# Kernel optimization log

Measured on AMD Instinct MI355X. Metric: run time of the kernel, lower is better.

Reference implementation:

```python
import jax, jax.numpy as jnp
import numpy as np

ALPHA = 1.702
LIMIT = 7.0

# Tiling: A*B*M = BD*S (total dispatched tokens)
A, B, E, M, H, I = 2, 8, 16, 128, 2048, 2048
_BD, _S = 2, 1024


def setup_inputs() -> dict:
    key = jax.random.key(0)
    ks = jax.random.split(key, 6)
    inv_h = 1.0 / np.sqrt(H)
    inv_i = 1.0 / np.sqrt(I)
    return {
        "dispatched": jax.random.normal(ks[0], (A, B, E, M, H), dtype=jnp.float32),
        "gate_up_proj": jax.random.normal(ks[1], (E, H, 2 * I), dtype=jnp.float32) * inv_h,
        "gate_up_proj_bias": jax.random.normal(ks[2], (E, 2 * I), dtype=jnp.float32) * 0.02,
        "down_proj": jax.random.normal(ks[3], (E, I, H), dtype=jnp.float32) * inv_i,
        "down_proj_bias": jax.random.normal(ks[4], (E, H), dtype=jnp.float32) * 0.02,
        "sparsity_remap": jax.random.randint(ks[5], (E, E), 0, E, dtype=jnp.int32),
        "BD": _BD,
        "S": _S,
    }


def _moe_activation_gpt_oss(gate_up_out):
    # interleaved gate/up: [g0,u0,g1,u1,...]
    gate = gate_up_out[..., ::2]
    up = gate_up_out[..., 1::2]
    gate = jnp.minimum(gate, LIMIT)
    up = jnp.clip(up, -LIMIT, LIMIT)
    glu = gate * jax.nn.sigmoid(gate * ALPHA)
    return (up + 1.0) * glu


def reference(dispatched, gate_up_proj, gate_up_proj_bias, down_proj,
              down_proj_bias, sparsity_remap, BD, S):
    # sparsity_remap is an opaque tile remap for tt.sparse_matmul; the dense
    # grouped matmul computes the same math (zero tiles contribute zeros).
    a, b, e, m, h = dispatched.shape
    inter = gate_up_proj.shape[-1] // 2
    # grouped gate_up GEMM: [A,B,E,M,H] @ [E,H,2I] -> [A,B,E,M,2I]
    gate_up_out = jnp.einsum('abemh,ehn->abemn', dispatched, gate_up_proj)
    gate_up_out = gate_up_out + gate_up_proj_bias[None, None, :, None, :]
    activated = _moe_activation_gpt_oss(gate_up_out)  # [A,B,E,M,I]
    activated = activated.reshape(a * b, e, m, inter)
    # grouped down GEMM: [AB,E,M,I] @ [E,I,H] -> [AB,E,M,H]
    down_out = jnp.einsum('xemi,eih->xemh', activated, down_proj)
    down_out = down_out + down_proj_bias[None, :, None, :]
    # untile: [AB,E,M,H] -> [AB,M,E,H] -> [BD,S,E,H]
    down_out = jnp.transpose(down_out, (0, 2, 1, 3))
    return down_out.reshape(BD, S, e, h)
```

## Files before the change

kernel.cpp:

```cpp
#include <hip/hip_runtime.h>
#include <stdint.h>

#define DEV __device__ __forceinline__

constexpr int E_ = 16, M_ = 128, H_ = 2048, I_ = 2048;
constexpr int X_ = 16;
constexpr int N1 = 2 * I_;
constexpr int ROWS = X_ * M_;

typedef short bfrag __attribute__((ext_vector_type(8)));
typedef float ffrag __attribute__((ext_vector_type(4)));
typedef unsigned short us8 __attribute__((ext_vector_type(8)));

DEV unsigned short f2bf(float f) {
    union { float f; unsigned u; } v; v.f = f;
    unsigned u = v.u;
    u += 0x7fffu + ((u >> 16) & 1u);
    return (unsigned short)(u >> 16);
}

DEV void gload16(const void* g, void* lds_wave_base) {
    __builtin_amdgcn_global_load_lds(
        (const __attribute__((address_space(1))) unsigned int*)g,
        (__attribute__((address_space(3))) unsigned int*)lds_wave_base,
        16, 0, 0);
}

DEV void block_bar() {
    asm volatile("" ::: "memory");
    __builtin_amdgcn_s_barrier();
    asm volatile("" ::: "memory");
}


__global__ __launch_bounds__(256) void convert_a(const float* __restrict__ in,
                                                 unsigned short* __restrict__ outb) {
    const int n4 = X_ * E_ * M_ * H_ / 4;
    int idx = blockIdx.x * 256 + threadIdx.x;
    int stride = gridDim.x * 256;
    for (int f = idx; f < n4; f += stride) {
        float4 v = ((const float4*)in)[f];
        ushort4 o;
        o.x = f2bf(v.x); o.y = f2bf(v.y); o.z = f2bf(v.z); o.w = f2bf(v.w);
        const int c = f & 511;
        const int row = f >> 9;
        const int m = row & 127, e = (row >> 7) & 15, x = row >> 11;
        ((ushort4*)outb)[((size_t)(e * ROWS + x * M_ + m) << 9) + c] = o;
    }
}

__global__ __launch_bounds__(256) void convert_b1(const float* __restrict__ gup,
                                                  unsigned short* __restrict__ b1t) {
    const int e = blockIdx.x, h0 = blockIdx.y * 64, n0 = blockIdx.z * 128;
    __shared__ float tile[64][129];
    const float* src = gup + (size_t)e * H_ * N1;
    const int t = threadIdx.x;
#pragma unroll
    for (int i = 0; i < 8; ++i) {
        int idx = i * 1024 + t * 4;
        int r = idx >> 7, c = idx & 127;
        float4 v = *(const float4*)(src + (size_t)(h0 + r) * N1 + n0 + c);
        tile[r][c] = v.x; tile[r][c + 1] = v.y; tile[r][c + 2] = v.z; tile[r][c + 3] = v.w;
    }
    __syncthreads();
    const int p = t >> 2;
    const int hh = (t & 3) * 16;
    us8 g0, g1, u0, u1;
#pragma unroll
    for (int k = 0; k < 8; ++k) {
        g0[k] = f2bf(tile[hh + k][2 * p]);
        u0[k] = f2bf(tile[hh + k][2 * p + 1]);
        g1[k] = f2bf(tile[hh + 8 + k][2 * p]);
        u1[k] = f2bf(tile[hh + 8 + k][2 * p + 1]);
    }
    unsigned short* dg = b1t + ((size_t)e * N1 + (n0 >> 1) + p) * H_ + h0 + hh;
    unsigned short* du = b1t + ((size_t)e * N1 + I_ + (n0 >> 1) + p) * H_ + h0 + hh;
    *(us8*)dg = g0; *(us8*)(dg + 8) = g1;
    *(us8*)du = u0; *(us8*)(du + 8) = u1;
}

__global__ __launch_bounds__(256) void convert_b2(const float* __restrict__ dwn,
                                                  unsigned short* __restrict__ b2t) {
    const int e = blockIdx.x, i0 = blockIdx.y * 64, h0 = blockIdx.z * 64;
    __shared__ float tile[64][65];
    const float* src = dwn + (size_t)e * I_ * H_;
    const int t = threadIdx.x;
#pragma unroll
    for (int it = 0; it < 4; ++it) {
        int idx = it * 1024 + t * 4;
        int r = idx >> 6, c = idx & 63;
        float4 v = *(const float4*)(src + (size_t)(i0 + r) * H_ + h0 + c);
        tile[r][c] = v.x; tile[r][c + 1] = v.y; tile[r][c + 2] = v.z; tile[r][c + 3] = v.w;
    }
    __syncthreads();
    const int hl = t >> 2, ii = (t & 3) * 16;
    us8 o0, o1;
#pragma unroll
    for (int k = 0; k < 8; ++k) {
        o0[k] = f2bf(tile[ii + k][hl]);
        o1[k] = f2bf(tile[ii + 8 + k][hl]);
    }
    unsigned short* d = b2t + ((size_t)e * H_ + h0 + hl) * I_ + i0 + ii;
    *(us8*)d = o0; *(us8*)(d + 8) = o1;
}

template <int MODE>
__global__ __launch_bounds__(512, 2) void gemm8p(
    const unsigned short* __restrict__ A,
    const unsigned short* __restrict__ B,
    const float* __restrict__ bias,
    void* __restrict__ outv)
{
    constexpr int LD = 2048;
    constexpr int BK = 32;
    constexpr int NT = 2048 / BK;

    __shared__ unsigned short lds[4][2][256 * BK];

    const int t = threadIdx.x, wave = t >> 6, lane = t & 63;
    const int wr = wave >> 2, wc = wave & 3;

    int id = blockIdx.x;
    const int cpx = gridDim.x >> 3;
    id = (id & 7) * cpx + (id >> 3);
    int e, mt, bt;
    if (MODE == 0) { e = id >> 7; mt = (id >> 4) & 7; bt = id & 15; }
    else           { e = id >> 6; mt = (id >> 3) & 7; bt = id & 7; }

    const unsigned short* Aexp = A + ((size_t)e * ROWS + mt * 256) * LD;
    const unsigned short* Bexp = (MODE == 0)
        ? B + (size_t)e * N1 * LD
        : B + ((size_t)e * H_ + bt * 256) * LD;

    ffrag acc[8][4];
#pragma unroll
    for (int i = 0; i < 8; ++i)
#pragma unroll
        for (int j = 0; j < 4; ++j) acc[i][j] = ffrag{0.f, 0.f, 0.f, 0.f};

    const int rsub = lane >> 2;
    const int csw = ((lane & 3) ^ ((lane >> 3) & 3)) * 8;

    auto stage = [&](int kt, int b) {
        const int k0 = kt * BK;
#pragma unroll
        for (int i = 0; i < 2; ++i) {
            const int Rb = (wave * 2 + i) * 16;
            const int r = Rb + rsub;
            gload16(Aexp + (size_t)r * LD + k0 + csw, (void*)&lds[b][0][Rb * BK]);
        }
#pragma unroll
        for (int i = 0; i < 2; ++i) {
            const int Rb = (wave * 2 + i) * 16;
            const int r = Rb + rsub;
            int grow;
            if (MODE == 0)
                grow = ((r >> 5) & 1) * I_ + bt * 128 + (r >> 6) * 32 + (r & 31);
            else
                grow = r;
            gload16(Bexp + (size_t)grow * LD + k0 + csw, (void*)&lds[b][1][Rb * BK]);
        }
    };

    const int l15 = lane & 15, lr16 = lane >> 4;
    const int swl = (l15 >> 1) & 3;
    const int kch = (lr16 ^ swl) * 8;
    const int arow0 = wr * 128 + l15;
    const int brow0 = wc * 64 + l15;

    bfrag bB_a[4], af_a[4], bB_b[4], af_b[4];

    stage(0, 0);
    stage(1, 1);
    stage(2, 2);
    asm volatile("s_waitcnt vmcnt(8)" ::: "memory");
    __builtin_amdgcn_sched_barrier(0);
    block_bar();
#pragma unroll
    for (int nf = 0; nf < 4; ++nf)
        bB_a[nf] = *(const bfrag*)&lds[0][1][(brow0 + nf * 16) * BK + kch];
#pragma unroll
    for (int mf = 0; mf < 4; ++mf)
        af_a[mf] = *(const bfrag*)&lds[0][0][(arow0 + mf * 16) * BK + kch];

#define TILE_BODY(KT_, BBC, A03C, BBN, A03N)                                     \
  {                                                                              \
    const int kt_ = (KT_);                                                       \
    const int cur_ = kt_ & 3;                                                    \
    asm volatile("s_waitcnt lgkmcnt(0)" ::: "memory");      \
    __builtin_amdgcn_sched_barrier(0);                                           \
    bfrag af47[4];                                                               \
    _Pragma("unroll")                                                            \
    for (int mf = 0; mf < 4; ++mf)                                               \
        af47[mf] = *(const bfrag*)&lds[cur_][0][(arow0 + (4 + mf) * 16) * BK + kch]; \
    __builtin_amdgcn_sched_barrier(0);                                           \
    __builtin_amdgcn_s_setprio(1);                                               \
    _Pragma("unroll")                                                            \
    for (int mf = 0; mf < 4; ++mf)                                               \
        _Pragma("unroll")                                                        \
        for (int nf = 0; nf < 4; ++nf)                                           \
            acc[mf][nf] = __builtin_amdgcn_mfma_f32_16x16x32_bf16(               \
                A03C[mf], BBC[nf], acc[mf][nf], 0, 0, 0);                        \
    __builtin_amdgcn_s_setprio(0);                                               \
    asm volatile("s_waitcnt lgkmcnt(0)" ::: "memory");          \
    __builtin_amdgcn_sched_barrier(0);                                           \
    if (kt_ + 1 < NT) {                                                          \
        if (kt_ + 2 < NT) { asm volatile("s_waitcnt vmcnt(4)" ::: "memory"); }   \
        else              { asm volatile("s_waitcnt vmcnt(0)" ::: "memory"); }   \
        __builtin_amdgcn_sched_barrier(0);                                       \
        block_bar();                             \
        if (kt_ + 3 < NT) stage(kt_ + 3, (kt_ + 3) & 3);                         \
        const int nxt_ = (kt_ + 1) & 3;                                          \
        _Pragma("unroll")                                                        \
        for (int nf = 0; nf < 4; ++nf)                                           \
            BBN[nf] = *(const bfrag*)&lds[nxt_][1][(brow0 + nf * 16) * BK + kch]; \
        _Pragma("unroll")                                                        \
        for (int mf = 0; mf < 4; ++mf)                                           \
            A03N[mf] = *(const bfrag*)&lds[nxt_][0][(arow0 + mf * 16) * BK + kch]; \
        __builtin_amdgcn_sched_barrier(0);                                       \
    }                                                                            \
    __builtin_amdgcn_s_setprio(1);                                               \
    _Pragma("unroll")                                                            \
    for (int mf = 0; mf < 4; ++mf)                                               \
        _Pragma("unroll")                                                        \
        for (int nf = 0; nf < 4; ++nf)                                           \
            acc[4 + mf][nf] = __builtin_amdgcn_mfma_f32_16x16x32_bf16(           \
                af47[mf], BBC[nf], acc[4 + mf][nf], 0, 0, 0);                    \
    __builtin_amdgcn_s_setprio(0);                                               \
  }

    for (int kt = 0; kt < NT; kt += 2) {
        TILE_BODY(kt,     bB_a, af_a, bB_b, af_b);
        TILE_BODY(kt + 1, bB_b, af_b, bB_a, af_a);
    }
#undef TILE_BODY

    const int rb = mt * 256 + wr * 128 + lr16 * 4;
    if (MODE == 0) {
        unsigned short* act = (unsigned short*)outv + (size_t)e * ROWS * I_;
#pragma unroll
        for (int nf = 0; nf < 2; ++nf) {
            const int jj = bt * 128 + wc * 32 + nf * 16 + l15;
            const float gb = bias[(size_t)e * N1 + 2 * jj];
            const float ub = bias[(size_t)e * N1 + 2 * jj + 1];
#pragma unroll
            for (int mf = 0; mf < 8; ++mf)
#pragma unroll
                for (int r = 0; r < 4; ++r) {
                    float g = acc[mf][nf][r] + gb;
                    float u = acc[mf][2 + nf][r] + ub;
                    g = fminf(g, 7.0f);
                    u = fminf(fmaxf(u, -7.0f), 7.0f);
                    const float glu = g / (1.0f + __expf(-1.702f * g));
                    const float av = (u + 1.0f) * glu;
                    act[(size_t)(rb + mf * 16 + r) * I_ + jj] = f2bf(av);
                }
        }
    } else {
        float* out = (float*)outv;
#pragma unroll
        for (int nf = 0; nf < 4; ++nf) {
            const int h = bt * 256 + wc * 64 + nf * 16 + l15;
            const float bb = bias[(size_t)e * H_ + h];
#pragma unroll
            for (int mf = 0; mf < 8; ++mf)
#pragma unroll
                for (int r = 0; r < 4; ++r) {
                    const int row = rb + mf * 16 + r;
                    out[((size_t)row * E_ + e) * H_ + h] = acc[mf][nf][r] + bb;
                }
        }
    }
}


extern "C" void kernel_launch(void* const* d_in, const int* in_sizes, int n_in,
                              void* d_out, int out_size, void* d_ws, size_t ws_size,
                              hipStream_t stream) {
    const float* disp  = (const float*)d_in[0];
    const float* gup   = (const float*)d_in[1];
    const float* gub   = (const float*)d_in[2];
    const float* down  = (const float*)d_in[3];
    const float* dbias = (const float*)d_in[4];
    float* out = (float*)d_out;

    const size_t NEED = (size_t)512 << 20;
    if (ws_size < NEED) {
        hipMemsetAsync(d_out, 0, (size_t)out_size * sizeof(float), stream);
        return;
    }
    unsigned short* a_bf = (unsigned short*)d_ws;
    unsigned short* b1t  = (unsigned short*)((char*)d_ws + ((size_t)128 << 20));
    unsigned short* b2t  = b1t;
    unsigned short* actb = (unsigned short*)((char*)d_ws + ((size_t)384 << 20));

    convert_a<<<4096, 256, 0, stream>>>(disp, a_bf);
    convert_b1<<<dim3(E_, H_ / 64, N1 / 128), 256, 0, stream>>>(gup, b1t);
    gemm8p<0><<<2048, 512, 0, stream>>>(a_bf, b1t, gub, actb);
    convert_b2<<<dim3(E_, I_ / 64, H_ / 64), 256, 0, stream>>>(down, b2t);
    gemm8p<1><<<1024, 512, 0, stream>>>(actb, b2t, dbias, out);
}
```

Before: 1.176 ms.

## Load A fragments directly from global, stage only B in LDS with BK=64

The GEMM mainloop stops staging the A operand through LDS. A fragments are now read straight from global memory into registers, and only B is staged, using a double buffer with a 64-wide K step and a new XOR swizzle. This removes the LDS traffic and capacity used for A and halves the number of K iterations and barriers. In exchange, A reads become uncoalesced direct global loads whose latency the pipeline has to hide, register pressure rises, and the prefetch depth drops from three stages to one.

```diff
diff --git a/kernel.cpp b/kernel.cpp
--- a/kernel.cpp
+++ b/kernel.cpp
@@ -112,10 +112,9 @@
     void* __restrict__ outv)
 {
     constexpr int LD = 2048;
-    constexpr int BK = 32;
-    constexpr int NT = 2048 / BK;
-
-    __shared__ unsigned short lds[4][2][256 * BK];
+    constexpr int NT = 2048 / 64;
+
+    __shared__ unsigned short lds[2][256 * 64];
 
     const int t = threadIdx.x, wave = t >> 6, lane = t & 63;
     const int wr = wave >> 2, wc = wave & 3;
@@ -138,100 +137,128 @@
 #pragma unroll
         for (int j = 0; j < 4; ++j) acc[i][j] = ffrag{0.f, 0.f, 0.f, 0.f};
 
-    const int rsub = lane >> 2;
-    const int csw = ((lane & 3) ^ ((lane >> 3) & 3)) * 8;
+    const int rsub = lane >> 3;
+    const int csw = ((lane & 7) ^ (lane >> 3)) * 8;
 
     auto stage = [&](int kt, int b) {
-        const int k0 = kt * BK;
-#pragma unroll
-        for (int i = 0; i < 2; ++i) {
-            const int Rb = (wave * 2 + i) * 16;
-            const int r = Rb + rsub;
-            gload16(Aexp + (size_t)r * LD + k0 + csw, (void*)&lds[b][0][Rb * BK]);
-        }
-#pragma unroll
-        for (int i = 0; i < 2; ++i) {
-            const int Rb = (wave * 2 + i) * 16;
+        const int k0 = kt * 64;
+#pragma unroll
+        for (int i = 0; i < 4; ++i) {
+            const int Rb = (wave * 4 + i) * 8;
             const int r = Rb + rsub;
             int grow;
             if (MODE == 0)
                 grow = ((r >> 5) & 1) * I_ + bt * 128 + (r >> 6) * 32 + (r & 31);
             else
                 grow = r;
-            gload16(Bexp + (size_t)grow * LD + k0 + csw, (void*)&lds[b][1][Rb * BK]);
+            gload16(Bexp + (size_t)grow * LD + k0 + csw, (void*)&lds[b][Rb * 64]);
         }
     };
 
-    const int l15 = lane & 15, lr16 = lane >> 4;
-    const int swl = (l15 >> 1) & 3;
-    const int kch = (lr16 ^ swl) * 8;
+    const int l15 = lane & 15, lr16 = lane >> 4, sw = lane & 7;
     const int arow0 = wr * 128 + l15;
     const int brow0 = wc * 64 + l15;
 
-    bfrag bB_a[4], af_a[4], bB_b[4], af_b[4];
+    const unsigned short* Arow = Aexp + (size_t)arow0 * LD + lr16 * 8;
+
+    bfrag afA[4][2], afB[4][2];
 
     stage(0, 0);
-    stage(1, 1);
-    stage(2, 2);
+#pragma unroll
+    for (int mf = 0; mf < 4; ++mf)
+#pragma unroll
+        for (int ks = 0; ks < 2; ++ks)
+            afA[mf][ks] = *(const bfrag*)(Arow + (size_t)(mf * 16) * LD + ks * 32);
     asm volatile("s_waitcnt vmcnt(8)" ::: "memory");
     __builtin_amdgcn_sched_barrier(0);
-    block_bar();
-#pragma unroll
-    for (int nf = 0; nf < 4; ++nf)
-        bB_a[nf] = *(const bfrag*)&lds[0][1][(brow0 + nf * 16) * BK + kch];
-#pragma unroll
-    for (int mf = 0; mf < 4; ++mf)
-        af_a[mf] = *(const bfrag*)&lds[0][0][(arow0 + mf * 16) * BK + kch];
-
-#define TILE_BODY(KT_, BBC, A03C, BBN, A03N)                                     \
+
+#define TILE_BODY(KT_, AFC, AFN)                                                 \
   {                                                                              \
     const int kt_ = (KT_);                                                       \
-    const int cur_ = kt_ & 3;                                                    \
-    asm volatile("s_waitcnt lgkmcnt(0)" ::: "memory");      \
-    __builtin_amdgcn_sched_barrier(0);                                           \
-    bfrag af47[4];                                                               \
-    _Pragma("unroll")                                                            \
-    for (int mf = 0; mf < 4; ++mf)                                               \
-        af47[mf] = *(const bfrag*)&lds[cur_][0][(arow0 + (4 + mf) * 16) * BK + kch]; \
+    const int cur_ = kt_ & 1;                                                    \
+    const int k0_ = kt_ * 64;                                                    \
+    block_bar();             \
+    bfrag bB0[2][2], bB1[2][2], ag[4][2];                                        \
+    _Pragma("unroll")                                                            \
+    for (int nf = 0; nf < 2; ++nf)                                               \
+        _Pragma("unroll")                                                        \
+        for (int ks = 0; ks < 2; ++ks)                                           \
+            bB0[nf][ks] = *(const bfrag*)&lds[cur_][(brow0 + nf * 16) * 64 + (((ks * 4 + lr16) ^ sw) * 8)]; \
+    asm volatile("" ::: "memory");                                               \
+    _Pragma("unroll")                                                            \
+    for (int nf = 0; nf < 2; ++nf)                                               \
+        _Pragma("unroll")                                                        \
+        for (int ks = 0; ks < 2; ++ks)                                           \
+            bB1[nf][ks] = *(const bfrag*)&lds[cur_][(brow0 + 32 + nf * 16) * 64 + (((ks * 4 + lr16) ^ sw) * 8)]; \
+    if (kt_ + 1 < NT) stage(kt_ + 1, cur_ ^ 1);                       \
+                                \
+    _Pragma("unroll")                                                            \
+    for (int mf = 0; mf < 4; ++mf)                                               \
+        _Pragma("unroll")                                                        \
+        for (int ks = 0; ks < 2; ++ks)                                           \
+            ag[mf][ks] = *(const bfrag*)(Arow + (size_t)(64 + mf * 16) * LD + k0_ + ks * 32); \
+                                                            \
+    asm volatile("s_waitcnt lgkmcnt(4)" ::: "memory");                           \
     __builtin_amdgcn_sched_barrier(0);                                           \
     __builtin_amdgcn_s_setprio(1);                                               \
     _Pragma("unroll")                                                            \
     for (int mf = 0; mf < 4; ++mf)                                               \
         _Pragma("unroll")                                                        \
-        for (int nf = 0; nf < 4; ++nf)                                           \
-            acc[mf][nf] = __builtin_amdgcn_mfma_f32_16x16x32_bf16(               \
-                A03C[mf], BBC[nf], acc[mf][nf], 0, 0, 0);                        \
+        for (int nf = 0; nf < 2; ++nf)                                           \
+            _Pragma("unroll")                                                    \
+            for (int ks = 0; ks < 2; ++ks)                                       \
+                acc[mf][nf] = __builtin_amdgcn_mfma_f32_16x16x32_bf16(           \
+                    AFC[mf][ks], bB0[nf][ks], acc[mf][nf], 0, 0, 0);             \
     __builtin_amdgcn_s_setprio(0);                                               \
-    asm volatile("s_waitcnt lgkmcnt(0)" ::: "memory");          \
+                                                            \
+    asm volatile("s_waitcnt lgkmcnt(0)" ::: "memory");                           \
     __builtin_amdgcn_sched_barrier(0);                                           \
+    __builtin_amdgcn_s_setprio(1);                                               \
+    _Pragma("unroll")                                                            \
+    for (int mf = 0; mf < 4; ++mf)                                               \
+        _Pragma("unroll")                                                        \
+        for (int nf = 0; nf < 2; ++nf)                                           \
+            _Pragma("unroll")                                                    \
+            for (int ks = 0; ks < 2; ++ks)                                       \
+                acc[mf][2 + nf] = __builtin_amdgcn_mfma_f32_16x16x32_bf16(       \
+                    AFC[mf][ks], bB1[nf][ks], acc[mf][2 + nf], 0, 0, 0);         \
+    __builtin_amdgcn_s_setprio(0);                                               \
+             \
     if (kt_ + 1 < NT) {                                                          \
-        if (kt_ + 2 < NT) { asm volatile("s_waitcnt vmcnt(4)" ::: "memory"); }   \
-        else              { asm volatile("s_waitcnt vmcnt(0)" ::: "memory"); }   \
-        __builtin_amdgcn_sched_barrier(0);                                       \
-        block_bar();                             \
-        if (kt_ + 3 < NT) stage(kt_ + 3, (kt_ + 3) & 3);                         \
-        const int nxt_ = (kt_ + 1) & 3;                                          \
-        _Pragma("unroll")                                                        \
-        for (int nf = 0; nf < 4; ++nf)                                           \
-            BBN[nf] = *(const bfrag*)&lds[nxt_][1][(brow0 + nf * 16) * BK + kch]; \
         _Pragma("unroll")                                                        \
         for (int mf = 0; mf < 4; ++mf)                                           \
-            A03N[mf] = *(const bfrag*)&lds[nxt_][0][(arow0 + mf * 16) * BK + kch]; \
-        __builtin_amdgcn_sched_barrier(0);                                       \
+            _Pragma("unroll")                                                    \
+            for (int ks = 0; ks < 2; ++ks)                                       \
+                AFN[mf][ks] = *(const bfrag*)(Arow + (size_t)(mf * 16) * LD + k0_ + 64 + ks * 32); \
+        asm volatile("s_waitcnt vmcnt(8)" ::: "memory");     \
+    } else {                                                                     \
+        asm volatile("s_waitcnt vmcnt(0)" ::: "memory");           \
     }                                                                            \
+    __builtin_amdgcn_sched_barrier(0);                                           \
+                                            \
     __builtin_amdgcn_s_setprio(1);                                               \
     _Pragma("unroll")                                                            \
     for (int mf = 0; mf < 4; ++mf)                                               \
         _Pragma("unroll")                                                        \
-        for (int nf = 0; nf < 4; ++nf)                                           \
-            acc[4 + mf][nf] = __builtin_amdgcn_mfma_f32_16x16x32_bf16(           \
-                af47[mf], BBC[nf], acc[4 + mf][nf], 0, 0, 0);                    \
+        for (int nf = 0; nf < 2; ++nf)                                           \
+            _Pragma("unroll")                                                    \
+            for (int ks = 0; ks < 2; ++ks)                                       \
+                acc[4 + mf][2 + nf] = __builtin_amdgcn_mfma_f32_16x16x32_bf16(   \
+                    ag[mf][ks], bB1[nf][ks], acc[4 + mf][2 + nf], 0, 0, 0);      \
+    _Pragma("unroll")                                                            \
+    for (int mf = 0; mf < 4; ++mf)                                               \
+        _Pragma("unroll")                                                        \
+        for (int nf = 0; nf < 2; ++nf)                                           \
+            _Pragma("unroll")                                                    \
+            for (int ks = 0; ks < 2; ++ks)                                       \
+                acc[4 + mf][nf] = __builtin_amdgcn_mfma_f32_16x16x32_bf16(       \
+                    ag[mf][ks], bB0[nf][ks], acc[4 + mf][nf], 0, 0, 0);          \
     __builtin_amdgcn_s_setprio(0);                                               \
   }
 
     for (int kt = 0; kt < NT; kt += 2) {
-        TILE_BODY(kt,     bB_a, af_a, bB_b, af_b);
-        TILE_BODY(kt + 1, bB_b, af_b, bB_a, af_a);
+        TILE_BODY(kt,     afA, afB);
+        TILE_BODY(kt + 1, afB, afA);
     }
 #undef TILE_BODY
 
```

Result: slower. 2.722 ms (+131.5%).
